# Optimization experiments

Measured on AMD Instinct MI355X. Metric: run time of the kernel, lower is better.

The kernel has to match this reference:

```python
import jax, jax.numpy as jnp
import numpy as np

B, T, E, H, DH = 8, 1024, 1024, 16, 64

def setup_inputs() -> dict:
    key = jax.random.key(0)
    ks = jax.random.split(key, 5)
    x = jax.random.normal(ks[0], (B, T, E), dtype=jnp.float32)
    Wq = jax.random.normal(ks[1], (H, E, DH), dtype=jnp.float32) * (E ** -0.5)
    Wk = jax.random.normal(ks[2], (H, E, DH), dtype=jnp.float32) * (E ** -0.5)
    Wv = jax.random.normal(ks[3], (H, E, DH), dtype=jnp.float32) * (E ** -0.5)
    Wp = jax.random.normal(ks[4], (E, E), dtype=jnp.float32) * (E ** -0.5)
    bp = jnp.zeros((E,), dtype=jnp.float32)
    return {"x": x, "Wq": Wq, "Wk": Wk, "Wv": Wv, "Wp": Wp, "bp": bp}

def reference(x, Wq, Wk, Wv, Wp, bp):
    # per-head projections (bias-free), vectorized over heads
    q = jnp.einsum('bte,hed->bhtd', x, Wq)
    k = jnp.einsum('bte,hed->bhtd', x, Wk)
    v = jnp.einsum('bte,hed->bhtd', x, Wv)
    scale = DH ** -0.5
    att = jnp.einsum('bhtd,bhsd->bhts', q, k) * scale  # [B,H,T,T]
    causal = jnp.tril(jnp.ones((T, T), dtype=bool))
    att = jnp.where(causal, att, -jnp.inf)
    att = jax.nn.softmax(att, axis=-1)
    # dropout is identity in eval mode
    out = jnp.einsum('bhts,bhsd->bhtd', att, v)
    out = out.transpose(0, 2, 1, 3).reshape(B, T, E)  # concat heads in order
    # proj: torch Linear y = x @ W^T + b
    out = out @ Wp.T + bp
    return out
```

## Files before the change

kernel.cpp:

```cpp
#include <hip/hip_runtime.h>

#define Bsz 8
#define Tsz 1024
#define Esz 1024
#define Hsz 16
#define DHsz 64
#define NQKV 3072

typedef _Float16 f16x8 __attribute__((ext_vector_type(8)));
typedef float f32x4 __attribute__((ext_vector_type(4)));
typedef unsigned short u16x8 __attribute__((ext_vector_type(8)));

__device__ __forceinline__ unsigned short f2h(float f) {
    union { _Float16 h; unsigned short u; } cv;
    cv.h = (_Float16)f;
    return cv.u;
}

__device__ __forceinline__ void async16(const void* g, void* l) {
    __builtin_amdgcn_global_load_lds(
        (const __attribute__((address_space(1))) void*)g,
        (__attribute__((address_space(3))) void*)l, 16, 0, 0);
}

#define MFMA(a, b, c) __builtin_amdgcn_mfma_f32_16x16x32_f16((a), (b), (c), 0, 0, 0)


__global__ void cast_f16_kernel(const float* __restrict__ in, unsigned short* __restrict__ outp) {
    int i = (blockIdx.x * 256 + threadIdx.x) * 4;
    float4 v = *(const float4*)(in + i);
    ushort4 o;
    o.x = f2h(v.x); o.y = f2h(v.y); o.z = f2h(v.z); o.w = f2h(v.w);
    *(ushort4*)(outp + i) = o;
}

__global__ __launch_bounds__(256) void pack_wqkv_kernel(
    const float* __restrict__ Wq, const float* __restrict__ Wk,
    const float* __restrict__ Wv, unsigned short* __restrict__ Bt) {
    __shared__ unsigned int tile[64 * 33];
    const int blk = blockIdx.x;
    const int et = blk & 15, h = (blk >> 4) & 15, which = blk >> 8;
    const int tid = threadIdx.x;
    const float* W = (which == 0) ? Wq : ((which == 1) ? Wk : Wv);
    const float* src = W + ((size_t)h * Esz + et * 64) * DHsz;
#pragma unroll
    for (int it = 0; it < 4; ++it) {
        int task = tid + it * 256;
        int er = task >> 4, ds = task & 15;
        float4 v = *(const float4*)(src + (size_t)er * DHsz + ds * 4);
        tile[er * 33 + ds * 2]     = (unsigned int)f2h(v.x) | ((unsigned int)f2h(v.y) << 16);
        tile[er * 33 + ds * 2 + 1] = (unsigned int)f2h(v.z) | ((unsigned int)f2h(v.w) << 16);
    }
    __syncthreads();
    unsigned short* dst = Bt + ((size_t)(which * 1024 + h * 64)) * Esz + et * 64;
#pragma unroll
    for (int it = 0; it < 2; ++it) {
        int task = tid + it * 256;
        int d = task & 63, es = task >> 6;
        int du = d >> 1, hi = d & 1;
        u16x8 v;
#pragma unroll
        for (int j = 0; j < 8; ++j) {
            unsigned int w = tile[(es * 8 + j) * 33 + du];
            v[j] = (unsigned short)(hi ? (w >> 16) : (w & 0xffffu));
        }
        *(u16x8*)(dst + (size_t)d * Esz + es * 8) = v;
    }
}

__global__ __launch_bounds__(256) void vtrans_kernel(const unsigned short* __restrict__ QKV,
                                                     unsigned short* __restrict__ VT) {
    __shared__ unsigned int tile[64 * 33];
    const int bh = blockIdx.x, tc = blockIdx.y;
    const int b = bh >> 4, h = bh & 15;
    const int tid = threadIdx.x;
    const unsigned short* src = QKV + ((size_t)(b * Tsz) + tc * 64) * NQKV + 2048 + h * 64;
#pragma unroll
    for (int it = 0; it < 2; ++it) {
        int task = tid + it * 256;
        int row = task >> 3, seg = task & 7;
        u16x8 v = *(const u16x8*)(src + (size_t)row * NQKV + seg * 8);
#pragma unroll
        for (int jj = 0; jj < 4; ++jj)
            tile[row * 33 + seg * 4 + jj] =
                (unsigned int)v[2 * jj] | ((unsigned int)v[2 * jj + 1] << 16);
    }
    __syncthreads();
    unsigned short* dst = VT + (size_t)bh * DHsz * Tsz + tc * 64;
#pragma unroll
    for (int it = 0; it < 2; ++it) {
        int task = tid + it * 256;
        int d = task & 63, tseg = task >> 6;
        int du = d >> 1, hi = d & 1;
        u16x8 v;
#pragma unroll
        for (int j = 0; j < 8; ++j) {
            unsigned int w = tile[(tseg * 8 + j) * 33 + du];
            v[j] = (unsigned short)(hi ? (w >> 16) : (w & 0xffffu));
        }
        *(u16x8*)(dst + (size_t)d * Tsz + tseg * 8) = v;
    }
}

template <int MODE>
__global__ __launch_bounds__(256, 4) void gemm_bt(
    const unsigned short* __restrict__ A,
    const unsigned short* __restrict__ Bt,
    int K, int N,
    unsigned short* __restrict__ c16,
    float* __restrict__ outp, const float* __restrict__ bias)
{
    __shared__ unsigned short smem[17408];
    unsigned short* sA = smem;
    unsigned short* sB = smem + 4096;
    const int tid = threadIdx.x;
    const int wid = tid >> 6, lane = tid & 63;
    const int quad = lane >> 4, l16 = lane & 15;
    const int col0 = blockIdx.x * 128;
    const int row0 = blockIdx.y * 128;
    const int wm = (wid >> 1) * 64, wn = (wid & 1) * 64;

    const f32x4 zero4 = {0.f, 0.f, 0.f, 0.f};
    f32x4 acc[4][4];
#pragma unroll
    for (int i = 0; i < 4; ++i)
#pragma unroll
        for (int j = 0; j < 4; ++j) acc[i][j] = zero4;

    const unsigned short* gA = A + (size_t)row0 * K;
    const unsigned short* gB = Bt + (size_t)col0 * K;
    const int c0 = wid * 2;
    const int srw = lane >> 2;
    const int ssg = (lane & 3) * 8;

    for (int k0 = 0; k0 < K; k0 += 32) {
#pragma unroll
        for (int cc = 0; cc < 2; ++cc) {
            int c = c0 + cc;
            async16(gA + (size_t)(c * 16 + srw) * K + k0 + ssg, (void*)(sA + c * 512 + lane * 8));
            async16(gB + (size_t)(c * 16 + srw) * K + k0 + ssg, (void*)(sB + c * 512 + lane * 8));
        }
        __syncthreads();

        f16x8 af[4], bfr[4];
#pragma unroll
        for (int i = 0; i < 4; ++i)
            af[i] = *(const f16x8*)(sA + (wm + i * 16 + l16) * 32 + quad * 8);
#pragma unroll
        for (int j = 0; j < 4; ++j)
            bfr[j] = *(const f16x8*)(sB + (wn + j * 16 + l16) * 32 + quad * 8);
#pragma unroll
        for (int i = 0; i < 4; ++i)
#pragma unroll
            for (int j = 0; j < 4; ++j)
                acc[i][j] = MFMA(af[i], bfr[j], acc[i][j]);
        __syncthreads();
    }

    if (MODE == 0) {
#pragma unroll
        for (int i = 0; i < 4; ++i)
#pragma unroll
            for (int r = 0; r < 4; ++r) {
                int rowL = wm + i * 16 + quad * 4 + r;
                unsigned short* tr = smem + rowL * 136 + wn + l16;
#pragma unroll
                for (int j = 0; j < 4; ++j)
                    tr[j * 16] = f2h(acc[i][j][r]);
            }
        __syncthreads();
        unsigned short* ob = c16 + (size_t)row0 * N + col0;
#pragma unroll
        for (int it = 0; it < 8; ++it) {
            int rowG = wid * 32 + it * 4 + quad;
            u16x8 v = *(const u16x8*)(smem + rowG * 136 + l16 * 8);
            *(u16x8*)(ob + (size_t)rowG * N + l16 * 8) = v;
        }
    } else {
        float* ft = (float*)smem;
#pragma unroll
        for (int p = 0; p < 2; ++p) {
            __syncthreads();
            if ((wid >> 1) == p) {
#pragma unroll
                for (int i = 0; i < 4; ++i)
#pragma unroll
                    for (int r = 0; r < 4; ++r) {
                        int rowL = i * 16 + quad * 4 + r;
                        float* tr = ft + rowL * 136 + wn + l16;
#pragma unroll
                        for (int j = 0; j < 4; ++j)
                            tr[j * 16] = acc[i][j][r] + bias[col0 + wn + j * 16 + l16];
                    }
            }
            __syncthreads();
#pragma unroll
            for (int it = 0; it < 8; ++it) {
                int task = tid + it * 256;
                int rowL = task >> 5, cs = task & 31;
                float4 v = *(const float4*)(ft + rowL * 136 + cs * 4);
                *(float4*)(outp + (size_t)(row0 + p * 64 + rowL) * N + col0 + cs * 4) = v;
            }
        }
    }
}

__global__ __launch_bounds__(256, 6) void attn_kernel(
    const unsigned short* __restrict__ QKV,
    const unsigned short* __restrict__ VTg,
    unsigned short* __restrict__ AO)
{
    const int bh = blockIdx.x;
    const int pair = blockIdx.y;
    const int b = bh >> 4, h = bh & 15;
    const int tid = threadIdx.x, wid = tid >> 6, lane = tid & 63;
    const int quad = lane >> 4, l16 = lane & 15;

    __shared__ unsigned short sK[64 * 64];
    __shared__ unsigned short sVt[64 * 64];
    __shared__ unsigned short sP[64 * 72];

    const unsigned short* Qb = QKV + (size_t)(b * Tsz) * NQKV + h * 64;
    const unsigned short* Kb = QKV + (size_t)(b * Tsz) * NQKV + 1024 + h * 64;
    const unsigned short* VTb = VTg + (size_t)bh * DHsz * Tsz;

    const int srow = lane >> 3;
    const int sseg = lane & 7;
    const int slog = sseg ^ srow;
    const int r0 = wid * 16;

    const float C1 = 0.18033688f;
    const float C2 = -4.32808512f;
    const f32x4 zero4 = {0.f, 0.f, 0.f, 0.f};

    for (int half = 0; half < 2; ++half) {
        const int qt = (half == 0) ? (15 - pair) : pair;
        const int q0 = qt * 64;
        const int rowlo = q0 + wid * 16;
        const int prow0 = wid * 16;

        f16x8 qf[2];
#pragma unroll
        for (int kk = 0; kk < 2; ++kk)
            qf[kk] = *(const f16x8*)(Qb + (size_t)(rowlo + l16) * NQKV + kk * 32 + quad * 8);

        f32x4 o[4];
        float lp[4];
#pragma unroll
        for (int dt = 0; dt < 4; ++dt) o[dt] = zero4;
#pragma unroll
        for (int r = 0; r < 4; ++r) lp[r] = 0.f;

        const int nblk = qt + 1;
        for (int blk = 0; blk < nblk; ++blk) {
            const int s0 = blk * 64;
            __syncthreads();
#pragma unroll
            for (int ii = 0; ii < 2; ++ii) {
                int rr = r0 + ii * 8;
                async16(Kb + (size_t)(s0 + rr + srow) * NQKV + slog * 8,
                        (void*)(sK + rr * 64 + lane * 8));
                async16(VTb + (size_t)(rr + srow) * Tsz + s0 + slog * 8,
                        (void*)(sVt + rr * 64 + lane * 8));
            }
            __syncthreads();

            f32x4 sc[4];
#pragma unroll
            for (int ct = 0; ct < 4; ++ct) sc[ct] = zero4;
#pragma unroll
            for (int kk = 0; kk < 2; ++kk) {
                f16x8 kf[4];
#pragma unroll
                for (int ct = 0; ct < 4; ++ct)
                    kf[ct] = *(const f16x8*)(sK + (ct * 16 + l16) * 64 +
                                             (((kk * 4 + quad) ^ (l16 & 7)) * 8));
#pragma unroll
                for (int ct = 0; ct < 4; ++ct)
                    sc[ct] = MFMA(qf[kk], kf[ct], sc[ct]);
            }

            if (blk < nblk - 1) {
#pragma unroll
                for (int r = 0; r < 4; ++r) {
                    unsigned short* pr = sP + (prow0 + quad * 4 + r) * 72 + l16;
#pragma unroll
                    for (int ct = 0; ct < 4; ++ct) {
                        float p = exp2f(fmaf(sc[ct][r], C1, C2));
                        lp[r] += p;
                        pr[ct * 16] = f2h(p);
                    }
                }
            } else {
#pragma unroll
                for (int r = 0; r < 4; ++r) {
                    int qrow = rowlo + quad * 4 + r;
                    unsigned short* pr = sP + (prow0 + quad * 4 + r) * 72 + l16;
#pragma unroll
                    for (int ct = 0; ct < 4; ++ct) {
                        float p = exp2f(fmaf(sc[ct][r], C1, C2));
                        p = (s0 + ct * 16 + l16 > qrow) ? 0.f : p;
                        lp[r] += p;
                        pr[ct * 16] = f2h(p);
                    }
                }
            }

#pragma unroll
            for (int kk = 0; kk < 2; ++kk) {
                f16x8 pf, vf[4];
                pf = *(const f16x8*)(sP + (prow0 + l16) * 72 + kk * 32 + quad * 8);
#pragma unroll
                for (int dt = 0; dt < 4; ++dt)
                    vf[dt] = *(const f16x8*)(sVt + (dt * 16 + l16) * 64 +
                                             (((kk * 4 + quad) ^ (l16 & 7)) * 8));
#pragma unroll
                for (int dt = 0; dt < 4; ++dt)
                    o[dt] = MFMA(pf, vf[dt], o[dt]);
            }
        }

#pragma unroll
        for (int r = 0; r < 4; ++r) {
            float s = lp[r];
            s += __shfl_xor(s, 1, 64);
            s += __shfl_xor(s, 2, 64);
            s += __shfl_xor(s, 4, 64);
            s += __shfl_xor(s, 8, 64);
            float inv = 1.0f / s;
            unsigned short* orow = sP + (prow0 + quad * 4 + r) * 72 + l16;
#pragma unroll
            for (int dt = 0; dt < 4; ++dt)
                orow[dt * 16] = f2h(o[dt][r] * inv);
        }
#pragma unroll
        for (int it = 0; it < 2; ++it) {
            int r8 = it * 8 + srow;
            u16x8 v = *(const u16x8*)(sP + (prow0 + r8) * 72 + sseg * 8);
            *(u16x8*)(AO + ((size_t)(b * Tsz + q0 + wid * 16 + r8)) * Esz +
                      h * 64 + sseg * 8) = v;
        }
    }
}


extern "C" void kernel_launch(void* const* d_in, const int* in_sizes, int n_in,
                              void* d_out, int out_size, void* d_ws, size_t ws_size,
                              hipStream_t stream)
{
    const float* x  = (const float*)d_in[0];
    const float* Wq = (const float*)d_in[1];
    const float* Wk = (const float*)d_in[2];
    const float* Wv = (const float*)d_in[3];
    const float* Wp = (const float*)d_in[4];
    const float* bp = (const float*)d_in[5];
    float* out = (float*)d_out;

    char* ws = (char*)d_ws;
    unsigned short* xb   = (unsigned short*)(ws);
    unsigned short* wqkv = (unsigned short*)(ws + 16777216);
    unsigned short* wpb  = (unsigned short*)(ws + 23068672);
    unsigned short* qkv  = (unsigned short*)(ws + 25165824);
    unsigned short* ao   = (unsigned short*)(ws + 75497472);
    unsigned short* vtb  = xb;

    cast_f16_kernel<<<8192, 256, 0, stream>>>(x, xb);
    pack_wqkv_kernel<<<768, 256, 0, stream>>>(Wq, Wk, Wv, wqkv);
    cast_f16_kernel<<<1024, 256, 0, stream>>>(Wp, wpb);

    gemm_bt<0><<<dim3(24, 64), 256, 0, stream>>>(xb, wqkv, 1024, 3072,
                                                 qkv, nullptr, nullptr);

    vtrans_kernel<<<dim3(128, 16), 256, 0, stream>>>(qkv, vtb);

    attn_kernel<<<dim3(128, 8), 256, 0, stream>>>(qkv, vtb, ao);

    gemm_bt<1><<<dim3(8, 64), 256, 0, stream>>>(ao, wpb, 1024, 1024,
                                                nullptr, out, bp);
}
```

Before: 279.1 us.

## Double-buffer K/V tiles and keep P in registers with transposed scores

The attention kernel now runs 512 threads per block on 128-query tiles, with K and V^T tiles double-buffered in LDS so the next tile's async loads overlap compute. Scores are computed transposed (K as A operand), so the exponentiated probabilities feed directly into 16x16x16 MFMAs as register operands instead of making a round trip through shared memory. The softmax denominator reduction becomes two cross-quad shuffles, and fully unmasked tiles skip the causal compare. In exchange it uses more LDS per block and more waves per block, and relies on hand-written waitcnt and barrier ordering for correctness.

After: 248.2 us. 1.12x faster.

```diff
diff --git a/kernel.cpp b/kernel.cpp
--- a/kernel.cpp
+++ b/kernel.cpp
@@ -8,6 +8,7 @@
 #define NQKV 3072
 
 typedef _Float16 f16x8 __attribute__((ext_vector_type(8)));
+typedef _Float16 f16x4 __attribute__((ext_vector_type(4)));
 typedef float f32x4 __attribute__((ext_vector_type(4)));
 typedef unsigned short u16x8 __attribute__((ext_vector_type(8)));
 
@@ -17,13 +18,21 @@
     return cv.u;
 }
 
+__device__ __forceinline__ unsigned int pkh2(float a, float b) {
+    typedef __fp16 h16x2 __attribute__((ext_vector_type(2)));
+    union { h16x2 v; unsigned int u; } cv;
+    cv.v = __builtin_amdgcn_cvt_pkrtz(a, b);
+    return cv.u;
+}
+
 __device__ __forceinline__ void async16(const void* g, void* l) {
     __builtin_amdgcn_global_load_lds(
         (const __attribute__((address_space(1))) void*)g,
         (__attribute__((address_space(3))) void*)l, 16, 0, 0);
 }
 
-#define MFMA(a, b, c) __builtin_amdgcn_mfma_f32_16x16x32_f16((a), (b), (c), 0, 0, 0)
+#define MFMA(a, b, c)   __builtin_amdgcn_mfma_f32_16x16x32_f16((a), (b), (c), 0, 0, 0)
+#define MFMA16(a, b, c) __builtin_amdgcn_mfma_f32_16x16x16f16((a), (b), (c), 0, 0, 0)
 
 
 __global__ void cast_f16_kernel(const float* __restrict__ in, unsigned short* __restrict__ outp) {
@@ -205,7 +214,7 @@
     }
 }
 
-__global__ __launch_bounds__(256, 6) void attn_kernel(
+__global__ __launch_bounds__(512, 6) void attn_kernel(
     const unsigned short* __restrict__ QKV,
     const unsigned short* __restrict__ VTg,
     unsigned short* __restrict__ AO)
@@ -216,9 +225,9 @@
     const int tid = threadIdx.x, wid = tid >> 6, lane = tid & 63;
     const int quad = lane >> 4, l16 = lane & 15;
 
-    __shared__ unsigned short sK[64 * 64];
-    __shared__ unsigned short sVt[64 * 64];
-    __shared__ unsigned short sP[64 * 72];
+    __shared__ unsigned short smem[16384];
+#define SKb(bf) (smem + (bf) * 4096)
+#define SVb(bf) (smem + 8192 + (bf) * 4096)
 
     const unsigned short* Qb = QKV + (size_t)(b * Tsz) * NQKV + h * 64;
     const unsigned short* Kb = QKV + (size_t)(b * Tsz) * NQKV + 1024 + h * 64;
@@ -227,120 +236,122 @@
     const int srow = lane >> 3;
     const int sseg = lane & 7;
     const int slog = sseg ^ srow;
-    const int r0 = wid * 16;
+    const int r0 = wid * 8;
+    const int xk = l16 & 7;
 
     const float C1 = 0.18033688f;
     const float C2 = -4.32808512f;
     const f32x4 zero4 = {0.f, 0.f, 0.f, 0.f};
 
     for (int half = 0; half < 2; ++half) {
-        const int qt = (half == 0) ? (15 - pair) : pair;
-        const int q0 = qt * 64;
+        const int qt = (half == 0) ? (7 - pair) : pair;
+        const int q0 = qt * 128;
         const int rowlo = q0 + wid * 16;
-        const int prow0 = wid * 16;
+        const int qrow = rowlo + l16;
+        const int nblk = (q0 >> 6) + 2;
+
+        __syncthreads();
+        async16(Kb + (size_t)(r0 + srow) * NQKV + slog * 8, (void*)(SKb(0) + r0 * 64 + lane * 8));
+        async16(VTb + (size_t)(r0 + srow) * Tsz + slog * 8, (void*)(SVb(0) + r0 * 64 + lane * 8));
 
         f16x8 qf[2];
 #pragma unroll
         for (int kk = 0; kk < 2; ++kk)
-            qf[kk] = *(const f16x8*)(Qb + (size_t)(rowlo + l16) * NQKV + kk * 32 + quad * 8);
+            qf[kk] = *(const f16x8*)(Qb + (size_t)qrow * NQKV + kk * 32 + quad * 8);
 
         f32x4 o[4];
-        float lp[4];
+        float lp = 0.f;
 #pragma unroll
         for (int dt = 0; dt < 4; ++dt) o[dt] = zero4;
-#pragma unroll
-        for (int r = 0; r < 4; ++r) lp[r] = 0.f;
-
-        const int nblk = qt + 1;
+
         for (int blk = 0; blk < nblk; ++blk) {
             const int s0 = blk * 64;
-            __syncthreads();
-#pragma unroll
-            for (int ii = 0; ii < 2; ++ii) {
-                int rr = r0 + ii * 8;
-                async16(Kb + (size_t)(s0 + rr + srow) * NQKV + slog * 8,
-                        (void*)(sK + rr * 64 + lane * 8));
-                async16(VTb + (size_t)(rr + srow) * Tsz + s0 + slog * 8,
-                        (void*)(sVt + rr * 64 + lane * 8));
-            }
-            __syncthreads();
-
-            f32x4 sc[4];
-#pragma unroll
-            for (int ct = 0; ct < 4; ++ct) sc[ct] = zero4;
+            const int cur = blk & 1;
+            __builtin_amdgcn_s_barrier();
+            if (blk + 1 < nblk) {
+                const int sn = (blk + 1) * 64;
+                async16(Kb + (size_t)(sn + r0 + srow) * NQKV + slog * 8,
+                        (void*)(SKb(cur ^ 1) + r0 * 64 + lane * 8));
+                async16(VTb + (size_t)(r0 + srow) * Tsz + sn + slog * 8,
+                        (void*)(SVb(cur ^ 1) + r0 * 64 + lane * 8));
+                __asm__ volatile("s_waitcnt vmcnt(2)" ::: "memory");
+            } else {
+                __asm__ volatile("s_waitcnt vmcnt(0)" ::: "memory");
+            }
+            __builtin_amdgcn_s_barrier();
+            __asm__ volatile("" ::: "memory");
+
+            if (s0 > rowlo + 15) continue;
+
+            f32x4 scT[4];
+#pragma unroll
+            for (int ct = 0; ct < 4; ++ct) scT[ct] = zero4;
 #pragma unroll
             for (int kk = 0; kk < 2; ++kk) {
-                f16x8 kf[4];
-#pragma unroll
-                for (int ct = 0; ct < 4; ++ct)
-                    kf[ct] = *(const f16x8*)(sK + (ct * 16 + l16) * 64 +
-                                             (((kk * 4 + quad) ^ (l16 & 7)) * 8));
-#pragma unroll
-                for (int ct = 0; ct < 4; ++ct)
-                    sc[ct] = MFMA(qf[kk], kf[ct], sc[ct]);
-            }
-
-            if (blk < nblk - 1) {
+#pragma unroll
+                for (int ct = 0; ct < 4; ++ct) {
+                    f16x8 kf = *(const f16x8*)(SKb(cur) + (ct * 16 + l16) * 64 +
+                                               (((kk * 4 + quad) ^ xk) * 8));
+                    scT[ct] = MFMA(kf, qf[kk], scT[ct]);
+                }
+            }
+
+            f16x4 pk[4];
+            const bool full = (s0 + 63 <= rowlo);
+#pragma unroll
+            for (int ct = 0; ct < 4; ++ct) {
+                int sb = s0 + ct * 16 + quad * 4;
+                float p[4];
 #pragma unroll
                 for (int r = 0; r < 4; ++r) {
-                    unsigned short* pr = sP + (prow0 + quad * 4 + r) * 72 + l16;
-#pragma unroll
-                    for (int ct = 0; ct < 4; ++ct) {
-                        float p = exp2f(fmaf(sc[ct][r], C1, C2));
-                        lp[r] += p;
-                        pr[ct * 16] = f2h(p);
-                    }
+                    float v = exp2f(fmaf(scT[ct][r], C1, C2));
+                    if (!full) v = (sb + r > qrow) ? 0.f : v;
+                    p[r] = v;
+                    lp += v;
                 }
-            } else {
-#pragma unroll
-                for (int r = 0; r < 4; ++r) {
-                    int qrow = rowlo + quad * 4 + r;
-                    unsigned short* pr = sP + (prow0 + quad * 4 + r) * 72 + l16;
-#pragma unroll
-                    for (int ct = 0; ct < 4; ++ct) {
-                        float p = exp2f(fmaf(sc[ct][r], C1, C2));
-                        p = (s0 + ct * 16 + l16 > qrow) ? 0.f : p;
-                        lp[r] += p;
-                        pr[ct * 16] = f2h(p);
-                    }
+                union { f16x4 v; unsigned int u[2]; } cv;
+                cv.u[0] = pkh2(p[0], p[1]);
+                cv.u[1] = pkh2(p[2], p[3]);
+                pk[ct] = cv.v;
+            }
+
+#pragma unroll
+            for (int ct = 0; ct < 4; ++ct) {
+                const int sl = 2 * ct + (quad >> 1);
+#pragma unroll
+                for (int dt = 0; dt < 4; ++dt) {
+                    f16x4 vf = *(const f16x4*)(SVb(cur) + (dt * 16 + l16) * 64 +
+                                               ((sl ^ xk) * 8) + (quad & 1) * 4);
+                    o[dt] = MFMA16(vf, pk[ct], o[dt]);
                 }
             }
-
-#pragma unroll
-            for (int kk = 0; kk < 2; ++kk) {
-                f16x8 pf, vf[4];
-                pf = *(const f16x8*)(sP + (prow0 + l16) * 72 + kk * 32 + quad * 8);
-#pragma unroll
-                for (int dt = 0; dt < 4; ++dt)
-                    vf[dt] = *(const f16x8*)(sVt + (dt * 16 + l16) * 64 +
-                                             (((kk * 4 + quad) ^ (l16 & 7)) * 8));
-#pragma unroll
-                for (int dt = 0; dt < 4; ++dt)
-                    o[dt] = MFMA(pf, vf[dt], o[dt]);
-            }
-        }
-
-#pragma unroll
-        for (int r = 0; r < 4; ++r) {
-            float s = lp[r];
-            s += __shfl_xor(s, 1, 64);
-            s += __shfl_xor(s, 2, 64);
-            s += __shfl_xor(s, 4, 64);
-            s += __shfl_xor(s, 8, 64);
-            float inv = 1.0f / s;
-            unsigned short* orow = sP + (prow0 + quad * 4 + r) * 72 + l16;
-#pragma unroll
-            for (int dt = 0; dt < 4; ++dt)
-                orow[dt * 16] = f2h(o[dt][r] * inv);
-        }
+        }
+
+        float s = lp;
+        s += __shfl_xor(s, 16, 64);
+        s += __shfl_xor(s, 32, 64);
+        float inv = 1.0f / s;
+
+        __syncthreads();
+        unsigned short* otr = smem;
+        const int orow = wid * 16 + l16;
+#pragma unroll
+        for (int dt = 0; dt < 4; ++dt) {
+            *(unsigned int*)(otr + orow * 72 + dt * 16 + quad * 4) =
+                pkh2(o[dt][0] * inv, o[dt][1] * inv);
+            *(unsigned int*)(otr + orow * 72 + dt * 16 + quad * 4 + 2) =
+                pkh2(o[dt][2] * inv, o[dt][3] * inv);
+        }
+        __syncthreads();
 #pragma unroll
         for (int it = 0; it < 2; ++it) {
-            int r8 = it * 8 + srow;
-            u16x8 v = *(const u16x8*)(sP + (prow0 + r8) * 72 + sseg * 8);
-            *(u16x8*)(AO + ((size_t)(b * Tsz + q0 + wid * 16 + r8)) * Esz +
-                      h * 64 + sseg * 8) = v;
-        }
-    }
+            int rr = wid * 16 + it * 8 + srow;
+            u16x8 v = *(const u16x8*)(otr + rr * 72 + sseg * 8);
+            *(u16x8*)(AO + (size_t)(b * Tsz + q0 + rr) * Esz + h * 64 + sseg * 8) = v;
+        }
+    }
+#undef SKb
+#undef SVb
 }
 
 
@@ -373,7 +384,7 @@
 
     vtrans_kernel<<<dim3(128, 16), 256, 0, stream>>>(qkv, vtb);
 
-    attn_kernel<<<dim3(128, 8), 256, 0, stream>>>(qkv, vtb, ao);
+    attn_kernel<<<dim3(128, 4), 512, 0, stream>>>(qkv, vtb, ao);
 
     gemm_bt<1><<<dim3(8, 64), 256, 0, stream>>>(ao, wpb, 1024, 1024,
                                                 nullptr, out, bp);
```
